# Kernel tuning notes

Hardware: AMD Instinct MI355X
Metric: run time of the kernel (lower is better)

Reference implementation:

```python
import jax, jax.numpy as jnp
import numpy as np

D_MODEL = 1024
D_CODEX = 64
CODEX_SIZE = 8192
BETA = 1.0
EPS_NORM = 1e-12
EPS_LN = 1e-5


def l2norm(x):
    # F.normalize(p=2, dim=-1, eps=1e-12): x / max(||x||, eps)
    n = jnp.sqrt(jnp.sum(x * x, axis=-1, keepdims=True))
    return x / jnp.maximum(n, EPS_NORM)


def setup_inputs() -> dict:
    key = jax.random.key(0)
    ks = jax.random.split(key, 8)
    B, S = 4, 2048
    Z = jax.random.normal(ks[0], (B, S, D_MODEL), dtype=jnp.float32)
    W1 = 0.02 * jax.random.normal(ks[1], (D_MODEL, D_MODEL), dtype=jnp.float32)
    b1 = jnp.zeros((D_MODEL,), dtype=jnp.float32)
    W2 = 0.02 * jax.random.normal(ks[2], (D_MODEL, D_CODEX), dtype=jnp.float32)
    b2 = jnp.zeros((D_CODEX,), dtype=jnp.float32)
    codex = l2norm(jax.random.normal(ks[3], (CODEX_SIZE, D_CODEX), dtype=jnp.float32))
    ln_w = jnp.ones((D_CODEX,), dtype=jnp.float32)
    ln_b = jnp.zeros((D_CODEX,), dtype=jnp.float32)
    Wp = 0.02 * jax.random.normal(ks[4], (D_CODEX, D_MODEL), dtype=jnp.float32)
    bp = jnp.zeros((D_MODEL,), dtype=jnp.float32)
    return {"Z": Z, "W1": W1, "b1": b1, "W2": W2, "b2": b2,
            "codex": codex, "ln_w": ln_w, "ln_b": ln_b, "Wp": Wp, "bp": bp}


def reference(Z, W1, b1, W2, b2, codex, ln_w, ln_b, Wp, bp):
    # pre_proj: Linear -> Tanh -> Linear, then l2-normalize into codex space
    Z_e = jnp.tanh(Z @ W1 + b1) @ W2 + b2            # (B, S, d_codex)
    Z_e = l2norm(Z_e)
    flat = Z_e.reshape(-1, D_CODEX)                  # (N, d_codex)
    # squared-L2 distances: |z|^2 + |c|^2 - 2 z.c
    dists = (jnp.sum(flat * flat, axis=-1, keepdims=True)
             + jnp.sum(codex * codex, axis=-1)[None, :]
             - 2.0 * jnp.einsum('nd,cd->nc', flat, codex))  # (N, K)
    idxs = jnp.argmin(dists, axis=-1).reshape(Z_e.shape[:-1])  # (B, S)
    codex_probs = jax.nn.one_hot(idxs, CODEX_SIZE, dtype=Z_e.dtype)  # (B, S, K)
    Z_q = codex[idxs]                                 # (B, S, d_codex)
    # commitment loss (codex is an EMA buffer, no gradient through it)
    loss = BETA * jnp.mean((jax.lax.stop_gradient(Z_q) - Z_e) ** 2)
    # straight-through estimator
    Z_q = Z_e + jax.lax.stop_gradient(Z_q - Z_e)
    # layernorm over d_codex
    mu = jnp.mean(Z_q, axis=-1, keepdims=True)
    var = jnp.mean((Z_q - mu) ** 2, axis=-1, keepdims=True)
    Z_q = (Z_q - mu) * jax.lax.rsqrt(var + EPS_LN) * ln_w + ln_b
    # post_proj back to d_model
    Z_q = Z_q @ Wp + bp                               # (B, S, d_model)
    return Z_q, loss, codex_probs
```

## Files before the change

### kernel.cpp

```cpp
#include <hip/hip_runtime.h>
#include <math.h>
#include <stdint.h>

#define N_TOK   8192
#define DMODEL  1024
#define DCODEX  64
#define KCODES  8192

typedef short short8 __attribute__((ext_vector_type(8)));
typedef _Float16 half8 __attribute__((ext_vector_type(8)));
typedef float f32x16 __attribute__((ext_vector_type(16)));
typedef float f32x4  __attribute__((ext_vector_type(4)));

union Frag  { short8 s; uint2 u[2]; };
union FragH { half8  h; uint2 u[2]; };
union H16   { _Float16 h; unsigned short s; };

__device__ __forceinline__ unsigned short f2bf(float f) {
    unsigned u = __float_as_uint(f);
    unsigned r = u + 0x7FFFu + ((u >> 16) & 1u);
    return (unsigned short)(r >> 16);
}
__device__ __forceinline__ float bf2f(unsigned short h) {
    return __uint_as_float(((unsigned)h) << 16);
}

__global__ __launch_bounds__(256) void codenorm_kernel(const float* __restrict__ codex,
                                                       float* __restrict__ cn2) {
    int k = blockIdx.x * 256 + threadIdx.x;
    const float4* p = (const float4*)(codex + (size_t)k * DCODEX);
    float s = 0.f;
#pragma unroll
    for (int i = 0; i < 16; ++i) {
        float4 v = p[i];
        s += v.x * v.x + v.y * v.y + v.z * v.z + v.w * v.w;
    }
    cn2[k] = s;
}

__global__ __launch_bounds__(256) void split3_kernel(const float* __restrict__ src,
                                                     unsigned short* __restrict__ p0,
                                                     unsigned short* __restrict__ p1,
                                                     unsigned short* __restrict__ p2) {
    size_t i4 = ((size_t)blockIdx.x * 256 + threadIdx.x) * 4;
    float4 v = *(const float4*)(src + i4);
    float f[4] = {v.x, v.y, v.z, v.w};
    ushort4 h0, h1, h2;
#pragma unroll
    for (int c = 0; c < 4; ++c) {
        unsigned short a0 = f2bf(f[c]);
        float r1 = f[c] - bf2f(a0);
        unsigned short a1 = f2bf(r1);
        float r2 = r1 - bf2f(a1);
        unsigned short a2 = f2bf(r2);
        ((unsigned short*)&h0)[c] = a0;
        ((unsigned short*)&h1)[c] = a1;
        ((unsigned short*)&h2)[c] = a2;
    }
    *(ushort4*)(p0 + i4) = h0;
    *(ushort4*)(p1 + i4) = h1;
    *(ushort4*)(p2 + i4) = h2;
}

__global__ __launch_bounds__(256) void split2h_kernel(const float* __restrict__ src,
                                                      unsigned short* __restrict__ p0,
                                                      unsigned short* __restrict__ p1) {
    size_t i4 = ((size_t)blockIdx.x * 256 + threadIdx.x) * 4;
    float4 v = *(const float4*)(src + i4);
    float f[4] = {v.x, v.y, v.z, v.w};
    ushort4 h0, h1;
#pragma unroll
    for (int c = 0; c < 4; ++c) {
        H16 a0, a1;
        a0.h = (_Float16)f[c];
        float r = f[c] - (float)a0.h;
        a1.h = (_Float16)r;
        ((unsigned short*)&h0)[c] = a0.s;
        ((unsigned short*)&h1)[c] = a1.s;
    }
    *(ushort4*)(p0 + i4) = h0;
    *(ushort4*)(p1 + i4) = h1;
}

__global__ __launch_bounds__(256) void split_w1_kernel(const float* __restrict__ W1,
                                                       unsigned short* __restrict__ t0,
                                                       unsigned short* __restrict__ t1,
                                                       unsigned short* __restrict__ t2) {
    __shared__ float tile[32][33];
    const int tid = threadIdx.x;
    const int k0 = blockIdx.x * 32;
    const int n0 = blockIdx.y * 32;
    {
        int i = tid >> 3, j4 = (tid & 7) * 4;
        float4 v = *(const float4*)(W1 + (size_t)(k0 + i) * DMODEL + n0 + j4);
        tile[i][j4 + 0] = v.x; tile[i][j4 + 1] = v.y;
        tile[i][j4 + 2] = v.z; tile[i][j4 + 3] = v.w;
    }
    __syncthreads();
    int n = tid >> 3, kq = (tid & 7) * 4;
    ushort4 h0, h1, h2;
#pragma unroll
    for (int c = 0; c < 4; ++c) {
        float f = tile[kq + c][n];
        unsigned short a0 = f2bf(f);
        float r1 = f - bf2f(a0);
        unsigned short a1 = f2bf(r1);
        float r2 = r1 - bf2f(a1);
        unsigned short a2 = f2bf(r2);
        ((unsigned short*)&h0)[c] = a0;
        ((unsigned short*)&h1)[c] = a1;
        ((unsigned short*)&h2)[c] = a2;
    }
    size_t off = (size_t)(n0 + n) * DMODEL + k0 + kq;
    *(ushort4*)(t0 + off) = h0;
    *(ushort4*)(t1 + off) = h1;
    *(ushort4*)(t2 + off) = h2;
}

__global__ __launch_bounds__(256) void gemm1_mfma_kernel(const unsigned short* __restrict__ Zt0,
                                                         const unsigned short* __restrict__ Zt1,
                                                         const unsigned short* __restrict__ Zt2,
                                                         const unsigned short* __restrict__ W1t0,
                                                         const unsigned short* __restrict__ W1t1,
                                                         const unsigned short* __restrict__ W1t2,
                                                         const float* __restrict__ b1,
                                                         float* __restrict__ H) {
    __shared__ unsigned short Ash[3][128][36];
    __shared__ unsigned short Bsh[3][128][36];
    const int tid = threadIdx.x;
    const int row0 = blockIdx.x * 128;
    const int col0 = blockIdx.y * 128;
    const int wave = tid >> 6;
    const int lane = tid & 63;
    const int lrow = lane & 31;
    const int lhalf = lane >> 5;
    const int wm = wave >> 1, wn = wave & 1;

    const unsigned short* Ap[3] = {Zt0, Zt1, Zt2};
    const unsigned short* Bp[3] = {W1t0, W1t1, W1t2};

    f32x16 acc[2][2];
#pragma unroll
    for (int i = 0; i < 2; ++i)
#pragma unroll
        for (int j = 0; j < 2; ++j)
#pragma unroll
            for (int r = 0; r < 16; ++r) acc[i][j][r] = 0.f;

    for (int k0 = 0; k0 < DMODEL; k0 += 32) {
        __syncthreads();
#pragma unroll
        for (int l = 0; l < 3; ++l) {
#pragma unroll
            for (int t = 0; t < 2; ++t) {
                int q = tid + t * 256;
                int r = q >> 2, kq = (q & 3) * 8;
                uint4 va = *(const uint4*)(Ap[l] + (size_t)(row0 + r) * DMODEL + k0 + kq);
                *(uint2*)&Ash[l][r][kq]     = make_uint2(va.x, va.y);
                *(uint2*)&Ash[l][r][kq + 4] = make_uint2(va.z, va.w);
                uint4 vb = *(const uint4*)(Bp[l] + (size_t)(col0 + r) * DMODEL + k0 + kq);
                *(uint2*)&Bsh[l][r][kq]     = make_uint2(vb.x, vb.y);
                *(uint2*)&Bsh[l][r][kq + 4] = make_uint2(vb.z, vb.w);
            }
        }
        __syncthreads();
#pragma unroll
        for (int mk = 0; mk < 2; ++mk) {
            const int kb = mk * 16 + lhalf * 8;
            Frag ah[2], am[2], al[2], bh[2], bm[2], bl[2];
#pragma unroll
            for (int ti = 0; ti < 2; ++ti) {
                int rA = wm * 64 + ti * 32 + lrow;
                ah[ti].u[0] = *(const uint2*)&Ash[0][rA][kb];
                ah[ti].u[1] = *(const uint2*)&Ash[0][rA][kb + 4];
                am[ti].u[0] = *(const uint2*)&Ash[1][rA][kb];
                am[ti].u[1] = *(const uint2*)&Ash[1][rA][kb + 4];
                al[ti].u[0] = *(const uint2*)&Ash[2][rA][kb];
                al[ti].u[1] = *(const uint2*)&Ash[2][rA][kb + 4];
            }
#pragma unroll
            for (int tj = 0; tj < 2; ++tj) {
                int rB = wn * 64 + tj * 32 + lrow;
                bh[tj].u[0] = *(const uint2*)&Bsh[0][rB][kb];
                bh[tj].u[1] = *(const uint2*)&Bsh[0][rB][kb + 4];
                bm[tj].u[0] = *(const uint2*)&Bsh[1][rB][kb];
                bm[tj].u[1] = *(const uint2*)&Bsh[1][rB][kb + 4];
                bl[tj].u[0] = *(const uint2*)&Bsh[2][rB][kb];
                bl[tj].u[1] = *(const uint2*)&Bsh[2][rB][kb + 4];
            }
#pragma unroll
            for (int ti = 0; ti < 2; ++ti)
#pragma unroll
                for (int tj = 0; tj < 2; ++tj) {
                    acc[ti][tj] = __builtin_amdgcn_mfma_f32_32x32x16_bf16(ah[ti].s, bh[tj].s, acc[ti][tj], 0, 0, 0);
                    acc[ti][tj] = __builtin_amdgcn_mfma_f32_32x32x16_bf16(ah[ti].s, bm[tj].s, acc[ti][tj], 0, 0, 0);
                    acc[ti][tj] = __builtin_amdgcn_mfma_f32_32x32x16_bf16(am[ti].s, bh[tj].s, acc[ti][tj], 0, 0, 0);
                    acc[ti][tj] = __builtin_amdgcn_mfma_f32_32x32x16_bf16(am[ti].s, bm[tj].s, acc[ti][tj], 0, 0, 0);
                    acc[ti][tj] = __builtin_amdgcn_mfma_f32_32x32x16_bf16(ah[ti].s, bl[tj].s, acc[ti][tj], 0, 0, 0);
                    acc[ti][tj] = __builtin_amdgcn_mfma_f32_32x32x16_bf16(al[ti].s, bh[tj].s, acc[ti][tj], 0, 0, 0);
                }
        }
    }

    float b1v[2];
#pragma unroll
    for (int tj = 0; tj < 2; ++tj) b1v[tj] = b1[col0 + wn * 64 + tj * 32 + lrow];
#pragma unroll
    for (int ti = 0; ti < 2; ++ti)
#pragma unroll
        for (int tj = 0; tj < 2; ++tj) {
            int col = col0 + wn * 64 + tj * 32 + lrow;
#pragma unroll
            for (int r = 0; r < 16; ++r) {
                int row = row0 + wm * 64 + ti * 32 + (r & 3) + 8 * (r >> 2) + 4 * lhalf;
                H[(size_t)row * DMODEL + col] = tanhf(acc[ti][tj][r] + b1v[tj]);
            }
        }
}

__global__ __launch_bounds__(256) void gemm2_norm_kernel(const float* __restrict__ H,
                                                         const float* __restrict__ W2,
                                                         const float* __restrict__ b2,
                                                         float* __restrict__ Ze) {
    __shared__ float As[64][36];
    __shared__ float Bs[64][68];
    const int tid = threadIdx.x;
    const int row0 = blockIdx.x * 32;
    const int ty = tid >> 4, tx = tid & 15;

    float acc[2][4];
#pragma unroll
    for (int i = 0; i < 2; ++i)
#pragma unroll
        for (int j = 0; j < 4; ++j) acc[i][j] = 0.f;

    for (int k0 = 0; k0 < DMODEL; k0 += 64) {
        __syncthreads();
#pragma unroll
        for (int t = 0; t < 2; ++t) {
            int q = tid + t * 256;
            int r = q >> 4, k4 = (q & 15) * 4;
            float4 v = *(const float4*)(H + (size_t)(row0 + r) * DMODEL + k0 + k4);
            As[k4 + 0][r] = v.x; As[k4 + 1][r] = v.y;
            As[k4 + 2][r] = v.z; As[k4 + 3][r] = v.w;
        }
#pragma unroll
        for (int t = 0; t < 4; ++t) {
            int q = tid + t * 256;
            int kk = q >> 4, c4 = (q & 15) * 4;
            *(float4*)&Bs[kk][c4] = *(const float4*)(W2 + (size_t)(k0 + kk) * DCODEX + c4);
        }
        __syncthreads();
#pragma unroll
        for (int k = 0; k < 64; ++k) {
            float2 a = *(const float2*)&As[k][ty * 2];
            float4 b = *(const float4*)&Bs[k][tx * 4];
            float bw[4] = {b.x, b.y, b.z, b.w};
#pragma unroll
            for (int j = 0; j < 4; ++j) {
                acc[0][j] = fmaf(a.x, bw[j], acc[0][j]);
                acc[1][j] = fmaf(a.y, bw[j], acc[1][j]);
            }
        }
    }
    float4 b2v4 = *(const float4*)(b2 + tx * 4);
    float b2v[4] = {b2v4.x, b2v4.y, b2v4.z, b2v4.w};
#pragma unroll
    for (int i = 0; i < 2; ++i) {
        float e[4];
#pragma unroll
        for (int j = 0; j < 4; ++j) e[j] = acc[i][j] + b2v[j];
        float ss = e[0] * e[0] + e[1] * e[1] + e[2] * e[2] + e[3] * e[3];
        ss += __shfl_xor(ss, 8, 64);
        ss += __shfl_xor(ss, 4, 64);
        ss += __shfl_xor(ss, 2, 64);
        ss += __shfl_xor(ss, 1, 64);
        float nrm = fmaxf(sqrtf(ss), 1e-12f);
        float o[4];
#pragma unroll
        for (int j = 0; j < 4; ++j) o[j] = e[j] / nrm;
        *(float4*)(Ze + (size_t)(row0 + ty * 2 + i) * DCODEX + tx * 4) = *(float4*)&o[0];
    }
}

__device__ __forceinline__ unsigned fenc(float f) {
    unsigned u = __float_as_uint(f);
    return (u & 0x80000000u) ? ~u : (u | 0x80000000u);
}
__device__ __forceinline__ unsigned long long ullmin2(unsigned long long a,
                                                      unsigned long long b) {
    return a < b ? a : b;
}

__global__ __launch_bounds__(256) void dist_mfma_kernel(const unsigned short* __restrict__ Zh,
                                                        const unsigned short* __restrict__ Zm,
                                                        const unsigned short* __restrict__ Ch,
                                                        const unsigned short* __restrict__ Cm,
                                                        const float* __restrict__ cn2,
                                                        unsigned long long* __restrict__ gbest) {
    __shared__ unsigned short Ash[2][128][68];
    __shared__ unsigned short Bsh[2][128][68];
    __shared__ unsigned long long red[128];
    const int tid = threadIdx.x;
    const int row0 = blockIdx.x * 128;
    const int col0 = blockIdx.y * 128;
    const int wave = tid >> 6;
    const int lane = tid & 63;
    const int lrow = lane & 31;
    const int lhalf = lane >> 5;
    const int wm = wave >> 1, wn = wave & 1;

    const unsigned short* Ap[2] = {Zh, Zm};
    const unsigned short* Bp[2] = {Ch, Cm};

    if (tid < 128) red[tid] = 0xFFFFFFFFFFFFFFFFull;

#pragma unroll
    for (int l = 0; l < 2; ++l) {
#pragma unroll
        for (int t = 0; t < 4; ++t) {
            int q = tid + t * 256;
            int r = q >> 3, kq = (q & 7) * 8;
            uint4 va = *(const uint4*)(Ap[l] + (size_t)(row0 + r) * DCODEX + kq);
            *(uint2*)&Ash[l][r][kq]     = make_uint2(va.x, va.y);
            *(uint2*)&Ash[l][r][kq + 4] = make_uint2(va.z, va.w);
            uint4 vb = *(const uint4*)(Bp[l] + (size_t)(col0 + r) * DCODEX + kq);
            *(uint2*)&Bsh[l][r][kq]     = make_uint2(vb.x, vb.y);
            *(uint2*)&Bsh[l][r][kq + 4] = make_uint2(vb.z, vb.w);
        }
    }
    __syncthreads();

    f32x16 acc[2][2];
#pragma unroll
    for (int i = 0; i < 2; ++i)
#pragma unroll
        for (int j = 0; j < 2; ++j)
#pragma unroll
            for (int r = 0; r < 16; ++r) acc[i][j][r] = 0.f;

#pragma unroll
    for (int mk = 0; mk < 4; ++mk) {
        const int kb = mk * 16 + lhalf * 8;
        FragH a0[2], a1[2], b0[2], b1[2];
#pragma unroll
        for (int ti = 0; ti < 2; ++ti) {
            int rA = wm * 64 + ti * 32 + lrow;
            a0[ti].u[0] = *(const uint2*)&Ash[0][rA][kb];
            a0[ti].u[1] = *(const uint2*)&Ash[0][rA][kb + 4];
            a1[ti].u[0] = *(const uint2*)&Ash[1][rA][kb];
            a1[ti].u[1] = *(const uint2*)&Ash[1][rA][kb + 4];
        }
#pragma unroll
        for (int tj = 0; tj < 2; ++tj) {
            int rB = wn * 64 + tj * 32 + lrow;
            b0[tj].u[0] = *(const uint2*)&Bsh[0][rB][kb];
            b0[tj].u[1] = *(const uint2*)&Bsh[0][rB][kb + 4];
            b1[tj].u[0] = *(const uint2*)&Bsh[1][rB][kb];
            b1[tj].u[1] = *(const uint2*)&Bsh[1][rB][kb + 4];
        }
#pragma unroll
        for (int ti = 0; ti < 2; ++ti)
#pragma unroll
            for (int tj = 0; tj < 2; ++tj) {
                acc[ti][tj] = __builtin_amdgcn_mfma_f32_32x32x16_f16(a0[ti].h, b0[tj].h, acc[ti][tj], 0, 0, 0);
                acc[ti][tj] = __builtin_amdgcn_mfma_f32_32x32x16_f16(a0[ti].h, b1[tj].h, acc[ti][tj], 0, 0, 0);
                acc[ti][tj] = __builtin_amdgcn_mfma_f32_32x32x16_f16(a1[ti].h, b0[tj].h, acc[ti][tj], 0, 0, 0);
            }
    }

    float cnv[2];
#pragma unroll
    for (int tj = 0; tj < 2; ++tj) cnv[tj] = cn2[col0 + wn * 64 + tj * 32 + lrow];
#pragma unroll
    for (int ti = 0; ti < 2; ++ti) {
#pragma unroll
        for (int r = 0; r < 16; ++r) {
            int rloc = wm * 64 + ti * 32 + (r & 3) + 8 * (r >> 2) + 4 * lhalf;
            unsigned long long kmin = 0xFFFFFFFFFFFFFFFFull;
#pragma unroll
            for (int tj = 0; tj < 2; ++tj) {
                float dist = fmaf(-2.0f, acc[ti][tj][r], cnv[tj]);
                unsigned col = (unsigned)(col0 + wn * 64 + tj * 32 + lrow);
                unsigned long long key = ((unsigned long long)fenc(dist) << 32) | col;
                kmin = ullmin2(kmin, key);
            }
#pragma unroll
            for (int m = 1; m <= 16; m <<= 1)
                kmin = ullmin2(kmin, (unsigned long long)__shfl_xor((long long)kmin, m, 64));
            if (lrow == 0) atomicMin(&red[rloc], kmin);
        }
    }
    __syncthreads();
    if (tid < 128) atomicMin(&gbest[row0 + tid], red[tid]);
}

__global__ __launch_bounds__(256) void zero_scatter_kernel(const unsigned long long* __restrict__ gbest,
                                                           float* __restrict__ probs) {
    size_t g = (size_t)blockIdx.x * 256 + threadIdx.x;
    int row = (int)(g >> 11);
    int c4i = (int)(g & 2047);
    unsigned id = (unsigned)(gbest[row] & 0xFFFFFFFFull);
    f32x4 v = {0.f, 0.f, 0.f, 0.f};
    if ((id >> 2) == (unsigned)c4i) v[id & 3] = 1.0f;
    __builtin_nontemporal_store(v, (f32x4*)(probs + ((size_t)row << 13) + ((size_t)c4i << 2)));
}

__global__ __launch_bounds__(256) void ln_loss_kernel(const unsigned long long* __restrict__ gbest,
                                                      const float* __restrict__ codex,
                                                      const float* __restrict__ Ze,
                                                      const float* __restrict__ ln_w,
                                                      const float* __restrict__ ln_b,
                                                      float* __restrict__ Aln,
                                                      float* __restrict__ loss) {
    const int tid = threadIdx.x;
    const int w = tid >> 6, l = tid & 63;
    const int row = blockIdx.x * 4 + w;
    int id = (int)(unsigned)(gbest[row] & 0xFFFFFFFFull);
    float zq = codex[(size_t)id * DCODEX + l];
    float ze = Ze[(size_t)row * DCODEX + l];
    float dlt = zq - ze;
    float val = ze + dlt;
    float s = val;
#pragma unroll
    for (int m = 32; m >= 1; m >>= 1) s += __shfl_xor(s, m, 64);
    float mu = s * 0.015625f;
    float c = val - mu;
    float v2 = c * c;
#pragma unroll
    for (int m = 32; m >= 1; m >>= 1) v2 += __shfl_xor(v2, m, 64);
    float var = v2 * 0.015625f;
    float y = c * (1.0f / sqrtf(var + 1e-5f)) * ln_w[l] + ln_b[l];
    Aln[(size_t)row * DCODEX + l] = y;
    float d2 = dlt * dlt;
#pragma unroll
    for (int m = 32; m >= 1; m >>= 1) d2 += __shfl_xor(d2, m, 64);
    if (l == 0) atomicAdd(loss, d2 * (1.0f / 524288.0f));
}

__global__ __launch_bounds__(256) void gemm3_kernel(const float* __restrict__ Aln,
                                                    const float* __restrict__ Wp,
                                                    const float* __restrict__ bp,
                                                    float* __restrict__ Zq) {
    __shared__ float As[64][132];
    __shared__ float Bs[64][68];
    const int tid = threadIdx.x;
    const int row0 = blockIdx.x * 128;
    const int col0 = blockIdx.y * 64;
    const int ty = tid >> 4, tx = tid & 15;

#pragma unroll
    for (int t = 0; t < 8; ++t) {
        int q = tid + t * 256;
        int r = q >> 4, d4 = (q & 15) * 4;
        float4 v = *(const float4*)(Aln + (size_t)(row0 + r) * DCODEX + d4);
        As[d4 + 0][r] = v.x; As[d4 + 1][r] = v.y;
        As[d4 + 2][r] = v.z; As[d4 + 3][r] = v.w;
    }
#pragma unroll
    for (int t = 0; t < 4; ++t) {
        int q = tid + t * 256;
        int kk = q >> 4, c4 = (q & 15) * 4;
        *(float4*)&Bs[kk][c4] = *(const float4*)(Wp + (size_t)kk * DMODEL + col0 + c4);
    }
    __syncthreads();

    float acc[8][4];
#pragma unroll
    for (int i = 0; i < 8; ++i)
#pragma unroll
        for (int j = 0; j < 4; ++j) acc[i][j] = 0.f;
#pragma unroll
    for (int k = 0; k < 64; ++k) {
        float a[8];
        *(float4*)&a[0] = *(const float4*)&As[k][ty * 4];
        *(float4*)&a[4] = *(const float4*)&As[k][64 + ty * 4];
        float4 b = *(const float4*)&Bs[k][tx * 4];
        float bw[4] = {b.x, b.y, b.z, b.w};
#pragma unroll
        for (int i = 0; i < 8; ++i)
#pragma unroll
            for (int j = 0; j < 4; ++j)
                acc[i][j] = fmaf(a[i], bw[j], acc[i][j]);
    }
    float4 bp4 = *(const float4*)(bp + col0 + tx * 4);
    float bb[4] = {bp4.x, bp4.y, bp4.z, bp4.w};
#pragma unroll
    for (int half = 0; half < 2; ++half)
#pragma unroll
        for (int i = 0; i < 4; ++i) {
            int r = row0 + half * 64 + ty * 4 + i;
            float o[4];
#pragma unroll
            for (int j = 0; j < 4; ++j) o[j] = acc[half * 4 + i][j] + bb[j];
            *(float4*)(Zq + (size_t)r * DMODEL + col0 + tx * 4) = *(float4*)&o[0];
        }
}

extern "C" void kernel_launch(void* const* d_in, const int* in_sizes, int n_in,
                              void* d_out, int out_size, void* d_ws, size_t ws_size,
                              hipStream_t stream) {
    const float* Z     = (const float*)d_in[0];
    const float* W1    = (const float*)d_in[1];
    const float* b1    = (const float*)d_in[2];
    const float* W2    = (const float*)d_in[3];
    const float* b2    = (const float*)d_in[4];
    const float* codex = (const float*)d_in[5];
    const float* ln_w  = (const float*)d_in[6];
    const float* ln_b  = (const float*)d_in[7];
    const float* Wp    = (const float*)d_in[8];
    const float* bp    = (const float*)d_in[9];

    float* out      = (float*)d_out;
    float* Zq_out   = out;
    float* loss_out = out + (size_t)N_TOK * DMODEL;
    float* probs    = loss_out + 1;

    char* ws = (char*)d_ws;
    float* H   = (float*)ws;
    float* Aln = H;
    float* Ze  = H + (size_t)N_TOK * DMODEL;
    float* cn2 = Ze + (size_t)N_TOK * DCODEX;
    unsigned long long* gbest = (unsigned long long*)(cn2 + KCODES);
    unsigned short* W1t0 = (unsigned short*)(gbest + N_TOK);
    unsigned short* W1t1 = W1t0 + (size_t)DMODEL * DMODEL;
    unsigned short* W1t2 = W1t1 + (size_t)DMODEL * DMODEL;
    unsigned short* Zt0  = W1t2 + (size_t)DMODEL * DMODEL;
    unsigned short* Zt1  = Zt0 + (size_t)N_TOK * DMODEL;
    unsigned short* Zt2  = Zt1 + (size_t)N_TOK * DMODEL;
    unsigned short* Zeh  = Zt2 + (size_t)N_TOK * DMODEL;
    unsigned short* Zem  = Zeh + (size_t)N_TOK * DCODEX;
    unsigned short* Cxh  = Zem + (size_t)N_TOK * DCODEX;
    unsigned short* Cxm  = Cxh + (size_t)KCODES * DCODEX;

    hipMemsetAsync(loss_out, 0, sizeof(float), stream);
    hipMemsetAsync(gbest, 0xFF, (size_t)N_TOK * sizeof(unsigned long long), stream);

    codenorm_kernel<<<KCODES / 256, 256, 0, stream>>>(codex, cn2);
    split_w1_kernel<<<dim3(DMODEL / 32, DMODEL / 32), 256, 0, stream>>>(W1, W1t0, W1t1, W1t2);
    split3_kernel<<<(int)(((size_t)N_TOK * DMODEL) / 1024), 256, 0, stream>>>(Z, Zt0, Zt1, Zt2);
    split2h_kernel<<<(int)(((size_t)KCODES * DCODEX) / 1024), 256, 0, stream>>>(codex, Cxh, Cxm);
    gemm1_mfma_kernel<<<dim3(N_TOK / 128, DMODEL / 128), 256, 0, stream>>>(Zt0, Zt1, Zt2, W1t0, W1t1, W1t2, b1, H);
    gemm2_norm_kernel<<<N_TOK / 32, 256, 0, stream>>>(H, W2, b2, Ze);
    split2h_kernel<<<(int)(((size_t)N_TOK * DCODEX) / 1024), 256, 0, stream>>>(Ze, Zeh, Zem);
    dist_mfma_kernel<<<dim3(N_TOK / 128, KCODES / 128), 256, 0, stream>>>(Zeh, Zem, Cxh, Cxm, cn2, gbest);
    zero_scatter_kernel<<<(int)(((size_t)N_TOK * KCODES / 4) / 256), 256, 0, stream>>>(gbest, probs);
    ln_loss_kernel<<<N_TOK / 4, 256, 0, stream>>>(gbest, codex, Ze, ln_w, ln_b, Aln, loss_out);
    gemm3_kernel<<<dim3(N_TOK / 128, DMODEL / 64), 256, 0, stream>>>(Aln, Wp, bp, Zq_out);
}
```

Before: 731.4 us.

## Switch GEMM1 to 2-way fp16 split and fuse split/norm kernels

```diff
diff --git a/kernel.cpp b/kernel.cpp
--- a/kernel.cpp
+++ b/kernel.cpp
@@ -7,60 +7,12 @@
 #define DCODEX  64
 #define KCODES  8192
 
-typedef short short8 __attribute__((ext_vector_type(8)));
 typedef _Float16 half8 __attribute__((ext_vector_type(8)));
 typedef float f32x16 __attribute__((ext_vector_type(16)));
 typedef float f32x4  __attribute__((ext_vector_type(4)));
 
-union Frag  { short8 s; uint2 u[2]; };
 union FragH { half8  h; uint2 u[2]; };
 union H16   { _Float16 h; unsigned short s; };
-
-__device__ __forceinline__ unsigned short f2bf(float f) {
-    unsigned u = __float_as_uint(f);
-    unsigned r = u + 0x7FFFu + ((u >> 16) & 1u);
-    return (unsigned short)(r >> 16);
-}
-__device__ __forceinline__ float bf2f(unsigned short h) {
-    return __uint_as_float(((unsigned)h) << 16);
-}
-
-__global__ __launch_bounds__(256) void codenorm_kernel(const float* __restrict__ codex,
-                                                       float* __restrict__ cn2) {
-    int k = blockIdx.x * 256 + threadIdx.x;
-    const float4* p = (const float4*)(codex + (size_t)k * DCODEX);
-    float s = 0.f;
-#pragma unroll
-    for (int i = 0; i < 16; ++i) {
-        float4 v = p[i];
-        s += v.x * v.x + v.y * v.y + v.z * v.z + v.w * v.w;
-    }
-    cn2[k] = s;
-}
-
-__global__ __launch_bounds__(256) void split3_kernel(const float* __restrict__ src,
-                                                     unsigned short* __restrict__ p0,
-                                                     unsigned short* __restrict__ p1,
-                                                     unsigned short* __restrict__ p2) {
-    size_t i4 = ((size_t)blockIdx.x * 256 + threadIdx.x) * 4;
-    float4 v = *(const float4*)(src + i4);
-    float f[4] = {v.x, v.y, v.z, v.w};
-    ushort4 h0, h1, h2;
-#pragma unroll
-    for (int c = 0; c < 4; ++c) {
-        unsigned short a0 = f2bf(f[c]);
-        float r1 = f[c] - bf2f(a0);
-        unsigned short a1 = f2bf(r1);
-        float r2 = r1 - bf2f(a1);
-        unsigned short a2 = f2bf(r2);
-        ((unsigned short*)&h0)[c] = a0;
-        ((unsigned short*)&h1)[c] = a1;
-        ((unsigned short*)&h2)[c] = a2;
-    }
-    *(ushort4*)(p0 + i4) = h0;
-    *(ushort4*)(p1 + i4) = h1;
-    *(ushort4*)(p2 + i4) = h2;
-}
 
 __global__ __launch_bounds__(256) void split2h_kernel(const float* __restrict__ src,
                                                       unsigned short* __restrict__ p0,
@@ -82,10 +34,38 @@
     *(ushort4*)(p1 + i4) = h1;
 }
 
+__global__ __launch_bounds__(256) void split2h_cn2_kernel(const float* __restrict__ src,
+                                                          unsigned short* __restrict__ p0,
+                                                          unsigned short* __restrict__ p1,
+                                                          float* __restrict__ cn2) {
+    const int tid = threadIdx.x;
+    size_t i4 = ((size_t)blockIdx.x * 256 + tid) * 4;
+    float4 v = *(const float4*)(src + i4);
+    float f[4] = {v.x, v.y, v.z, v.w};
+    ushort4 h0, h1;
+    float s = 0.f;
+#pragma unroll
+    for (int c = 0; c < 4; ++c) {
+        H16 a0, a1;
+        a0.h = (_Float16)f[c];
+        float r = f[c] - (float)a0.h;
+        a1.h = (_Float16)r;
+        ((unsigned short*)&h0)[c] = a0.s;
+        ((unsigned short*)&h1)[c] = a1.s;
+        s += f[c] * f[c];
+    }
+    *(ushort4*)(p0 + i4) = h0;
+    *(ushort4*)(p1 + i4) = h1;
+    s += __shfl_xor(s, 1, 64);
+    s += __shfl_xor(s, 2, 64);
+    s += __shfl_xor(s, 4, 64);
+    s += __shfl_xor(s, 8, 64);
+    if ((tid & 15) == 0) cn2[i4 >> 6] = s;
+}
+
 __global__ __launch_bounds__(256) void split_w1_kernel(const float* __restrict__ W1,
                                                        unsigned short* __restrict__ t0,
-                                                       unsigned short* __restrict__ t1,
-                                                       unsigned short* __restrict__ t2) {
+                                                       unsigned short* __restrict__ t1) {
     __shared__ float tile[32][33];
     const int tid = threadIdx.x;
     const int k0 = blockIdx.x * 32;
@@ -98,35 +78,30 @@
     }
     __syncthreads();
     int n = tid >> 3, kq = (tid & 7) * 4;
-    ushort4 h0, h1, h2;
+    ushort4 h0, h1;
 #pragma unroll
     for (int c = 0; c < 4; ++c) {
         float f = tile[kq + c][n];
-        unsigned short a0 = f2bf(f);
-        float r1 = f - bf2f(a0);
-        unsigned short a1 = f2bf(r1);
-        float r2 = r1 - bf2f(a1);
-        unsigned short a2 = f2bf(r2);
-        ((unsigned short*)&h0)[c] = a0;
-        ((unsigned short*)&h1)[c] = a1;
-        ((unsigned short*)&h2)[c] = a2;
+        H16 a0, a1;
+        a0.h = (_Float16)f;
+        float r = f - (float)a0.h;
+        a1.h = (_Float16)r;
+        ((unsigned short*)&h0)[c] = a0.s;
+        ((unsigned short*)&h1)[c] = a1.s;
     }
     size_t off = (size_t)(n0 + n) * DMODEL + k0 + kq;
     *(ushort4*)(t0 + off) = h0;
     *(ushort4*)(t1 + off) = h1;
-    *(ushort4*)(t2 + off) = h2;
-}
-
-__global__ __launch_bounds__(256) void gemm1_mfma_kernel(const unsigned short* __restrict__ Zt0,
-                                                         const unsigned short* __restrict__ Zt1,
-                                                         const unsigned short* __restrict__ Zt2,
-                                                         const unsigned short* __restrict__ W1t0,
-                                                         const unsigned short* __restrict__ W1t1,
-                                                         const unsigned short* __restrict__ W1t2,
+}
+
+__global__ __launch_bounds__(256) void gemm1_mfma_kernel(const unsigned short* __restrict__ Zh,
+                                                         const unsigned short* __restrict__ Zm,
+                                                         const unsigned short* __restrict__ W1h,
+                                                         const unsigned short* __restrict__ W1m,
                                                          const float* __restrict__ b1,
                                                          float* __restrict__ H) {
-    __shared__ unsigned short Ash[3][128][36];
-    __shared__ unsigned short Bsh[3][128][36];
+    __shared__ unsigned short Ash[2][128][36];
+    __shared__ unsigned short Bsh[2][128][36];
     const int tid = threadIdx.x;
     const int row0 = blockIdx.x * 128;
     const int col0 = blockIdx.y * 128;
@@ -136,8 +111,8 @@
     const int lhalf = lane >> 5;
     const int wm = wave >> 1, wn = wave & 1;
 
-    const unsigned short* Ap[3] = {Zt0, Zt1, Zt2};
-    const unsigned short* Bp[3] = {W1t0, W1t1, W1t2};
+    const unsigned short* Ap[2] = {Zh, Zm};
+    const unsigned short* Bp[2] = {W1h, W1m};
 
     f32x16 acc[2][2];
 #pragma unroll
@@ -150,7 +125,7 @@
     for (int k0 = 0; k0 < DMODEL; k0 += 32) {
         __syncthreads();
 #pragma unroll
-        for (int l = 0; l < 3; ++l) {
+        for (int l = 0; l < 2; ++l) {
 #pragma unroll
             for (int t = 0; t < 2; ++t) {
                 int q = tid + t * 256;
@@ -167,37 +142,30 @@
 #pragma unroll
         for (int mk = 0; mk < 2; ++mk) {
             const int kb = mk * 16 + lhalf * 8;
-            Frag ah[2], am[2], al[2], bh[2], bm[2], bl[2];
+            FragH a0[2], a1[2], b0[2], b1[2];
 #pragma unroll
             for (int ti = 0; ti < 2; ++ti) {
                 int rA = wm * 64 + ti * 32 + lrow;
-                ah[ti].u[0] = *(const uint2*)&Ash[0][rA][kb];
-                ah[ti].u[1] = *(const uint2*)&Ash[0][rA][kb + 4];
-                am[ti].u[0] = *(const uint2*)&Ash[1][rA][kb];
-                am[ti].u[1] = *(const uint2*)&Ash[1][rA][kb + 4];
-                al[ti].u[0] = *(const uint2*)&Ash[2][rA][kb];
-                al[ti].u[1] = *(const uint2*)&Ash[2][rA][kb + 4];
+                a0[ti].u[0] = *(const uint2*)&Ash[0][rA][kb];
+                a0[ti].u[1] = *(const uint2*)&Ash[0][rA][kb + 4];
+                a1[ti].u[0] = *(const uint2*)&Ash[1][rA][kb];
+                a1[ti].u[1] = *(const uint2*)&Ash[1][rA][kb + 4];
             }
 #pragma unroll
             for (int tj = 0; tj < 2; ++tj) {
                 int rB = wn * 64 + tj * 32 + lrow;
-                bh[tj].u[0] = *(const uint2*)&Bsh[0][rB][kb];
-                bh[tj].u[1] = *(const uint2*)&Bsh[0][rB][kb + 4];
-                bm[tj].u[0] = *(const uint2*)&Bsh[1][rB][kb];
-                bm[tj].u[1] = *(const uint2*)&Bsh[1][rB][kb + 4];
-                bl[tj].u[0] = *(const uint2*)&Bsh[2][rB][kb];
-                bl[tj].u[1] = *(const uint2*)&Bsh[2][rB][kb + 4];
+                b0[tj].u[0] = *(const uint2*)&Bsh[0][rB][kb];
+                b0[tj].u[1] = *(const uint2*)&Bsh[0][rB][kb + 4];
+                b1[tj].u[0] = *(const uint2*)&Bsh[1][rB][kb];
+                b1[tj].u[1] = *(const uint2*)&Bsh[1][rB][kb + 4];
             }
 #pragma unroll
             for (int ti = 0; ti < 2; ++ti)
 #pragma unroll
                 for (int tj = 0; tj < 2; ++tj) {
-                    acc[ti][tj] = __builtin_amdgcn_mfma_f32_32x32x16_bf16(ah[ti].s, bh[tj].s, acc[ti][tj], 0, 0, 0);
-                    acc[ti][tj] = __builtin_amdgcn_mfma_f32_32x32x16_bf16(ah[ti].s, bm[tj].s, acc[ti][tj], 0, 0, 0);
-                    acc[ti][tj] = __builtin_amdgcn_mfma_f32_32x32x16_bf16(am[ti].s, bh[tj].s, acc[ti][tj], 0, 0, 0);
-                    acc[ti][tj] = __builtin_amdgcn_mfma_f32_32x32x16_bf16(am[ti].s, bm[tj].s, acc[ti][tj], 0, 0, 0);
-                    acc[ti][tj] = __builtin_amdgcn_mfma_f32_32x32x16_bf16(ah[ti].s, bl[tj].s, acc[ti][tj], 0, 0, 0);
-                    acc[ti][tj] = __builtin_amdgcn_mfma_f32_32x32x16_bf16(al[ti].s, bh[tj].s, acc[ti][tj], 0, 0, 0);
+                    acc[ti][tj] = __builtin_amdgcn_mfma_f32_32x32x16_f16(a0[ti].h, b0[tj].h, acc[ti][tj], 0, 0, 0);
+                    acc[ti][tj] = __builtin_amdgcn_mfma_f32_32x32x16_f16(a0[ti].h, b1[tj].h, acc[ti][tj], 0, 0, 0);
+                    acc[ti][tj] = __builtin_amdgcn_mfma_f32_32x32x16_f16(a1[ti].h, b0[tj].h, acc[ti][tj], 0, 0, 0);
                 }
         }
     }
@@ -221,7 +189,9 @@
 __global__ __launch_bounds__(256) void gemm2_norm_kernel(const float* __restrict__ H,
                                                          const float* __restrict__ W2,
                                                          const float* __restrict__ b2,
-                                                         float* __restrict__ Ze) {
+                                                         float* __restrict__ Ze,
+                                                         unsigned short* __restrict__ Zeh,
+                                                         unsigned short* __restrict__ Zem) {
     __shared__ float As[64][36];
     __shared__ float Bs[64][68];
     const int tid = threadIdx.x;
@@ -277,9 +247,21 @@
         ss += __shfl_xor(ss, 1, 64);
         float nrm = fmaxf(sqrtf(ss), 1e-12f);
         float o[4];
-#pragma unroll
-        for (int j = 0; j < 4; ++j) o[j] = e[j] / nrm;
-        *(float4*)(Ze + (size_t)(row0 + ty * 2 + i) * DCODEX + tx * 4) = *(float4*)&o[0];
+        ushort4 h0, h1;
+#pragma unroll
+        for (int j = 0; j < 4; ++j) {
+            o[j] = e[j] / nrm;
+            H16 a0, a1;
+            a0.h = (_Float16)o[j];
+            float r = o[j] - (float)a0.h;
+            a1.h = (_Float16)r;
+            ((unsigned short*)&h0)[j] = a0.s;
+            ((unsigned short*)&h1)[j] = a1.s;
+        }
+        size_t off = (size_t)(row0 + ty * 2 + i) * DCODEX + tx * 4;
+        *(float4*)(Ze + off) = *(float4*)&o[0];
+        *(ushort4*)(Zeh + off) = h0;
+        *(ushort4*)(Zem + off) = h1;
     }
 }
 
@@ -522,27 +504,23 @@
     float* Ze  = H + (size_t)N_TOK * DMODEL;
     float* cn2 = Ze + (size_t)N_TOK * DCODEX;
     unsigned long long* gbest = (unsigned long long*)(cn2 + KCODES);
-    unsigned short* W1t0 = (unsigned short*)(gbest + N_TOK);
-    unsigned short* W1t1 = W1t0 + (size_t)DMODEL * DMODEL;
-    unsigned short* W1t2 = W1t1 + (size_t)DMODEL * DMODEL;
-    unsigned short* Zt0  = W1t2 + (size_t)DMODEL * DMODEL;
-    unsigned short* Zt1  = Zt0 + (size_t)N_TOK * DMODEL;
-    unsigned short* Zt2  = Zt1 + (size_t)N_TOK * DMODEL;
-    unsigned short* Zeh  = Zt2 + (size_t)N_TOK * DMODEL;
-    unsigned short* Zem  = Zeh + (size_t)N_TOK * DCODEX;
-    unsigned short* Cxh  = Zem + (size_t)N_TOK * DCODEX;
-    unsigned short* Cxm  = Cxh + (size_t)KCODES * DCODEX;
+    unsigned short* W1h = (unsigned short*)(gbest + N_TOK);
+    unsigned short* W1m = W1h + (size_t)DMODEL * DMODEL;
+    unsigned short* Zth = W1m + (size_t)DMODEL * DMODEL;
+    unsigned short* Ztm = Zth + (size_t)N_TOK * DMODEL;
+    unsigned short* Zeh = Ztm + (size_t)N_TOK * DMODEL;
+    unsigned short* Zem = Zeh + (size_t)N_TOK * DCODEX;
+    unsigned short* Cxh = Zem + (size_t)N_TOK * DCODEX;
+    unsigned short* Cxm = Cxh + (size_t)KCODES * DCODEX;
 
     hipMemsetAsync(loss_out, 0, sizeof(float), stream);
     hipMemsetAsync(gbest, 0xFF, (size_t)N_TOK * sizeof(unsigned long long), stream);
 
-    codenorm_kernel<<<KCODES / 256, 256, 0, stream>>>(codex, cn2);
-    split_w1_kernel<<<dim3(DMODEL / 32, DMODEL / 32), 256, 0, stream>>>(W1, W1t0, W1t1, W1t2);
-    split3_kernel<<<(int)(((size_t)N_TOK * DMODEL) / 1024), 256, 0, stream>>>(Z, Zt0, Zt1, Zt2);
-    split2h_kernel<<<(int)(((size_t)KCODES * DCODEX) / 1024), 256, 0, stream>>>(codex, Cxh, Cxm);
-    gemm1_mfma_kernel<<<dim3(N_TOK / 128, DMODEL / 128), 256, 0, stream>>>(Zt0, Zt1, Zt2, W1t0, W1t1, W1t2, b1, H);
-    gemm2_norm_kernel<<<N_TOK / 32, 256, 0, stream>>>(H, W2, b2, Ze);
-    split2h_kernel<<<(int)(((size_t)N_TOK * DCODEX) / 1024), 256, 0, stream>>>(Ze, Zeh, Zem);
+    split_w1_kernel<<<dim3(DMODEL / 32, DMODEL / 32), 256, 0, stream>>>(W1, W1h, W1m);
+    split2h_kernel<<<(int)(((size_t)N_TOK * DMODEL) / 1024), 256, 0, stream>>>(Z, Zth, Ztm);
+    split2h_cn2_kernel<<<(int)(((size_t)KCODES * DCODEX) / 1024), 256, 0, stream>>>(codex, Cxh, Cxm, cn2);
+    gemm1_mfma_kernel<<<dim3(N_TOK / 128, DMODEL / 128), 256, 0, stream>>>(Zth, Ztm, W1h, W1m, b1, H);
+    gemm2_norm_kernel<<<N_TOK / 32, 256, 0, stream>>>(H, W2, b2, Ze, Zeh, Zem);
     dist_mfma_kernel<<<dim3(N_TOK / 128, KCODES / 128), 256, 0, stream>>>(Zeh, Zem, Cxh, Cxm, cn2, gbest);
     zero_scatter_kernel<<<(int)(((size_t)N_TOK * KCODES / 4) / 256), 256, 0, stream>>>(gbest, probs);
     ln_loss_kernel<<<N_TOK / 4, 256, 0, stream>>>(gbest, codex, Ze, ln_w, ln_b, Aln, loss_out);
```

Result: faster. 685.0 us (-6.3%).
